# Performance work log

Hardware: AMD Instinct MI355X
Metric: run time of the kernel (lower is better)

Reference implementation:

```python
import jax, jax.numpy as jnp
import numpy as np

N_SEND = 49152   # 12 * 64^2 HEALPix nodes
N_REC = 65536    # 256x256 receiver grid
N_EDGES = 262144 # N_REC * 4 nearest senders
D_MODEL = 256
EDGE_IN, EDGE_OUT = 4, 64
LIN_IN, LIN_OUT = 320, 256
B = 2


def setup_inputs() -> dict:
    key = jax.random.key(0)
    ks = jax.random.split(key, 8)
    x = jax.random.normal(ks[0], (B, N_SEND, D_MODEL), dtype=jnp.float32)
    senders = jax.random.randint(ks[1], (N_EDGES,), 0, N_SEND, dtype=jnp.int32)
    receivers = jax.random.randint(ks[2], (N_EDGES,), 0, N_REC, dtype=jnp.int32)
    edge_index = jnp.stack([senders, receivers], axis=0)
    edge_attr = jax.random.normal(ks[3], (N_EDGES, EDGE_IN), dtype=jnp.float32)
    s = lambda fan_in: 1.0 / np.sqrt(fan_in)
    return {
        "x": x,
        "edge_index": edge_index,
        "edge_attr": edge_attr,
        "ee_w1": jax.random.normal(ks[4], (EDGE_IN, EDGE_OUT), dtype=jnp.float32) * s(EDGE_IN),
        "ee_b1": jnp.zeros((EDGE_OUT,), dtype=jnp.float32),
        "ee_w2": jax.random.normal(ks[5], (EDGE_OUT, EDGE_OUT), dtype=jnp.float32) * s(EDGE_OUT),
        "ee_b2": jnp.zeros((EDGE_OUT,), dtype=jnp.float32),
        "ff_w1": jax.random.normal(ks[6], (LIN_IN, LIN_OUT), dtype=jnp.float32) * s(LIN_IN),
        "ff_b1": jnp.zeros((LIN_OUT,), dtype=jnp.float32),
        "ff_w2": jax.random.normal(ks[7], (LIN_OUT, LIN_OUT), dtype=jnp.float32) * s(LIN_OUT),
        "ff_b2": jnp.zeros((LIN_OUT,), dtype=jnp.float32),
    }


def reference(x, edge_index, edge_attr,
              ee_w1, ee_b1, ee_w2, ee_b2,
              ff_w1, ff_b1, ff_w2, ff_b2):
    senders, receivers = edge_index[0], edge_index[1]
    # edge embedder MLP: [E, edge_in] -> [E, edge_out]
    h = jax.nn.relu(edge_attr @ ee_w1 + ee_b1)
    edge_feat = h @ ee_w2 + ee_b2                       # [E, edge_out]
    # gather sender node features: [B, E, d_model]
    v_s = x[:, senders, :]
    # concat with broadcast edge features: [B, E, d_model + edge_out]
    ef = jnp.broadcast_to(edge_feat[None], (x.shape[0],) + edge_feat.shape)
    v_s_prime = jnp.concatenate([v_s, ef], axis=-1)
    # scatter-sum onto receiver nodes: [B, n_rec, lin_in]
    v_m_sum = jnp.zeros((x.shape[0], N_REC, v_s_prime.shape[-1]), dtype=x.dtype)
    v_m_sum = v_m_sum.at[:, receivers, :].add(v_s_prime)
    # g2m feedforward: [B, n_rec, lin_out]
    h2 = jax.nn.relu(v_m_sum @ ff_w1 + ff_b1)
    return h2 @ ff_w2 + ff_b2
```

## Files before the change

### kernel.cpp

```cpp
#include <hip/hip_runtime.h>
#include <hip/hip_bf16.h>

#define N_SEND 49152
#define N_REC  65536
#define N_EDGES 262144
#define D_MODEL 256
#define EDGE_IN 4
#define EDGE_OUT 64
#define LIN_IN 320
#define LIN_OUT 256
#define BATCH 2

#define EPB 32
#define GBM 128

typedef __attribute__((ext_vector_type(4))) float f32x4;
typedef __attribute__((ext_vector_type(8))) short bf16x8;

static __device__ __forceinline__ unsigned short f2bf(float f) {
    union { float f; unsigned u; } v; v.f = f;
    unsigned r = v.u + 0x7FFF + ((v.u >> 16) & 1);
    return (unsigned short)(r >> 16);
}
static __device__ __forceinline__ float bf2f(unsigned short h) {
    union { unsigned u; float f; } v; v.u = ((unsigned)h) << 16; return v.f;
}

static __device__ __forceinline__ void async_copy16(void* lds_ptr, const void* g_ptr) {
    __builtin_amdgcn_global_load_lds(
        (const __attribute__((address_space(1))) void*)g_ptr,
        (__attribute__((address_space(3))) void*)lds_ptr, 16, 0, 0);
}

__global__ __launch_bounds__(256) void conv_x_kernel(
    const float* __restrict__ x, unsigned short* __restrict__ xb)
{
    const size_t i = ((size_t)blockIdx.x * 256 + threadIdx.x) * 8;
    const float4 v0 = *(const float4*)&x[i];
    const float4 v1 = *(const float4*)&x[i + 4];
    bf16x8 o;
    o[0] = (short)f2bf(v0.x); o[1] = (short)f2bf(v0.y);
    o[2] = (short)f2bf(v0.z); o[3] = (short)f2bf(v0.w);
    o[4] = (short)f2bf(v1.x); o[5] = (short)f2bf(v1.y);
    o[6] = (short)f2bf(v1.z); o[7] = (short)f2bf(v1.w);
    *(bf16x8*)&xb[i] = o;
}

__global__ __launch_bounds__(256) void edge_mlp_kernel(
    const int* __restrict__ receivers,
    const float* __restrict__ edge_attr,
    const float* __restrict__ ee_w1, const float* __restrict__ ee_b1,
    const float* __restrict__ ee_w2, const float* __restrict__ ee_b2,
    unsigned short* __restrict__ efs, int* __restrict__ counts)
{
    __shared__ float h_lds[EPB][EDGE_OUT];
    __shared__ float e_lds[EPB][EDGE_OUT];

    const int tid = threadIdx.x;
    const int e0 = blockIdx.x * EPB;

    if (tid < EPB) atomicAdd(&counts[receivers[e0 + tid]], 1);

    for (int i = tid; i < EPB * EDGE_OUT; i += 256) {
        const int e = i >> 6, j = i & 63;
        const float* ea = edge_attr + (size_t)(e0 + e) * EDGE_IN;
        float acc = ee_b1[j];
        acc += ea[0] * ee_w1[0 * EDGE_OUT + j];
        acc += ea[1] * ee_w1[1 * EDGE_OUT + j];
        acc += ea[2] * ee_w1[2 * EDGE_OUT + j];
        acc += ea[3] * ee_w1[3 * EDGE_OUT + j];
        h_lds[e][j] = fmaxf(acc, 0.0f);
    }
    __syncthreads();

    {
        const int j = tid & 63, g = tid >> 6;
        float acc[8];
#pragma unroll
        for (int e = 0; e < 8; ++e) acc[e] = ee_b2[j];
        for (int k = 0; k < EDGE_OUT; ++k) {
            const float w = ee_w2[k * EDGE_OUT + j];
#pragma unroll
            for (int e = 0; e < 8; ++e) acc[e] += h_lds[g * 8 + e][k] * w;
        }
#pragma unroll
        for (int e = 0; e < 8; ++e) e_lds[g * 8 + e][j] = acc[e];
    }
    __syncthreads();

    {
        const int e = tid >> 3, seg = tid & 7;
        const float* src = &e_lds[e][seg * 8];
        bf16x8 o;
#pragma unroll
        for (int j = 0; j < 8; ++j) o[j] = (short)f2bf(src[j]);
        *(bf16x8*)&efs[(size_t)(e0 + e) * EDGE_OUT + seg * 8] = o;
    }
}

__global__ __launch_bounds__(1024) void scan_kernel(
    const int* __restrict__ counts, int* __restrict__ row_ptr,
    int* __restrict__ cursor)
{
    __shared__ int sums[1024];
    const int t = threadIdx.x;
    const int4* c4 = (const int4*)(counts + t * 64);

    int s = 0;
#pragma unroll
    for (int i = 0; i < 16; ++i) { const int4 c = c4[i]; s += c.x + c.y + c.z + c.w; }
    sums[t] = s;
    __syncthreads();

    for (int off = 1; off < 1024; off <<= 1) {
        const int v = (t >= off) ? sums[t - off] : 0;
        __syncthreads();
        sums[t] += v;
        __syncthreads();
    }

    int run = sums[t] - s;
#pragma unroll
    for (int i = 0; i < 16; ++i) {
        const int4 c = c4[i];
        int4 w;
        w.x = run; w.y = run + c.x; w.z = w.y + c.y; w.w = w.z + c.z;
        run = w.w + c.w;
        ((int4*)(row_ptr + t * 64))[i] = w;
        ((int4*)(cursor + t * 64))[i] = w;
    }
    if (t == 1023) row_ptr[N_REC] = run;
}

__global__ __launch_bounds__(256) void fill_kernel(
    const int* __restrict__ senders, const int* __restrict__ receivers,
    int* __restrict__ cursor, int* __restrict__ edge_order,
    int* __restrict__ ssort)
{
    const int e = blockIdx.x * 256 + threadIdx.x;
    const int r = receivers[e];
    const int pos = atomicAdd(&cursor[r], 1);
    edge_order[pos] = e;
    ssort[pos] = senders[e];
}

template<bool XB>
__global__ __launch_bounds__(256) void gather_kernel(
    const float* __restrict__ x,
    const unsigned short* __restrict__ xb,
    const unsigned short* __restrict__ efs,
    const int* __restrict__ row_ptr,
    const int* __restrict__ edge_order,
    const int* __restrict__ ssort,
    unsigned short* __restrict__ vmb)
{
    const int lane = threadIdx.x & 63;
    const int wave = threadIdx.x >> 6;
    const int r = blockIdx.x * 4 + wave;
    const int beg = row_ptr[r], end = row_ptr[r + 1];
    const int half = lane >> 5, l2 = lane & 31;

    float ax[8] = {0, 0, 0, 0, 0, 0, 0, 0};
    float ae[8] = {0, 0, 0, 0, 0, 0, 0, 0};

    for (int chunk = beg; chunk < end; chunk += 64) {
        const int n = min(64, end - chunk);
        int myidx = 0, myeidx = 0;
        if (chunk + lane < end) {
            myidx = ssort[chunk + lane];
            myeidx = edge_order[chunk + lane];
        }
        for (int i = 0; i < n; ++i) {
            const int s = __shfl(myidx, i);
            const int e = __shfl(myeidx, i);
            const size_t rowbase = (size_t)(half ? N_SEND + s : s) * D_MODEL;
            if (XB) {
                const bf16x8 v = *(const bf16x8*)&xb[rowbase + l2 * 8];
#pragma unroll
                for (int j = 0; j < 8; ++j) ax[j] += bf2f((unsigned short)v[j]);
            } else {
                const float4 v0 = *(const float4*)&x[rowbase + l2 * 8];
                const float4 v1 = *(const float4*)&x[rowbase + l2 * 8 + 4];
                ax[0] += v0.x; ax[1] += v0.y; ax[2] += v0.z; ax[3] += v0.w;
                ax[4] += v1.x; ax[5] += v1.y; ax[6] += v1.z; ax[7] += v1.w;
            }
            if (lane < 8) {
                const bf16x8 w = *(const bf16x8*)&efs[(size_t)e * EDGE_OUT + lane * 8];
#pragma unroll
                for (int j = 0; j < 8; ++j) ae[j] += bf2f((unsigned short)w[j]);
            }
        }
    }

    bf16x8 o;
#pragma unroll
    for (int j = 0; j < 8; ++j) o[j] = (short)f2bf(ax[j]);
    *(bf16x8*)&vmb[((size_t)(half * N_REC + r)) * LIN_IN + l2 * 8] = o;
    if (lane < 8) {
        bf16x8 oe;
#pragma unroll
        for (int j = 0; j < 8; ++j) oe[j] = (short)f2bf(ae[j]);
        *(bf16x8*)&vmb[((size_t)r) * LIN_IN + D_MODEL + lane * 8] = oe;
        *(bf16x8*)&vmb[((size_t)(N_REC + r)) * LIN_IN + D_MODEL + lane * 8] = oe;
    }
}

__global__ __launch_bounds__(256) void prep_weights(
    const float* __restrict__ w1, const float* __restrict__ w2,
    unsigned short* __restrict__ w1t, unsigned short* __restrict__ w2t)
{
    const int tid = blockIdx.x * 256 + threadIdx.x;
    if (tid < 256 * LIN_IN) {
        const int n = tid / LIN_IN, k = tid - n * LIN_IN;
        w1t[tid] = f2bf(w1[k * LIN_OUT + n]);
    } else {
        const int t2 = tid - 256 * LIN_IN;
        if (t2 < 256 * 256) {
            const int n = t2 >> 8, k = t2 & 255;
            w2t[t2] = f2bf(w2[k * LIN_OUT + n]);
        }
    }
}

template<int K, bool IS_L1>
__global__ __launch_bounds__(512, 2) void gemm_node(
    const unsigned short* __restrict__ A,
    const unsigned short* __restrict__ BT,
    const float* __restrict__ bias,
    unsigned short* __restrict__ hout,
    float* __restrict__ fout)
{
    __shared__ __align__(16) char lds[49152];

    const int tid  = threadIdx.x;
    const int lane = tid & 63, wave = tid >> 6;
    const int n16  = lane & 15, hi = lane >> 4;
    const int wr   = wave >> 2, wc = wave & 3;
    const size_t row0 = (size_t)blockIdx.x * GBM;

    const int f_l = (n16 & 3) ^ ((n16 >> 2) & 3);
    const int hsl = (hi ^ f_l) << 4;

    auto stage = [&](int kk, int buf) {
        {
            const int i = tid, row = i >> 2;
            const int sl = (i & 3) ^ ((row & 3) ^ ((row >> 2) & 3));
            const unsigned short* g = A + (row0 + row) * LIN_IN + kk + sl * 8;
            char* l = lds + (buf << 13) + ((tid >> 6) << 10);
            async_copy16(l, g);
        }
#pragma unroll
        for (int p = 0; p < 2; ++p) {
            const int i = p * 512 + tid, row = i >> 2;
            const int sl = (i & 3) ^ ((row & 3) ^ ((row >> 2) & 3));
            const unsigned short* g = BT + (size_t)row * K + kk + sl * 8;
            char* l = lds + 16384 + (buf << 14) + (p << 13) + ((tid >> 6) << 10);
            async_copy16(l, g);
        }
    };

    f32x4 acc[4][4];
#pragma unroll
    for (int c = 0; c < 4; ++c) {
        const float bv = bias[64 * wc + 16 * c + n16];
#pragma unroll
        for (int t = 0; t < 4; ++t) {
            acc[t][c][0] = bv; acc[t][c][1] = bv; acc[t][c][2] = bv; acc[t][c][3] = bv;
        }
    }

    stage(0, 0);
    int cur = 0;
    const int NSTEP = K / 32;
    for (int step = 0; step < NSTEP; ++step) {
        if (step + 1 < NSTEP) stage((step + 1) * 32, cur ^ 1);
        __syncthreads();

        bf16x8 af[4], bf[4];
        const char* Ab = lds + (cur << 13);
        const char* Bb = lds + 16384 + (cur << 14);
#pragma unroll
        for (int t = 0; t < 4; ++t)
            af[t] = *(const bf16x8*)(Ab + (64 * wr + 16 * t + n16) * 64 + hsl);
#pragma unroll
        for (int c = 0; c < 4; ++c)
            bf[c] = *(const bf16x8*)(Bb + (64 * wc + 16 * c + n16) * 64 + hsl);
#pragma unroll
        for (int c = 0; c < 4; ++c)
#pragma unroll
            for (int t = 0; t < 4; ++t)
                acc[t][c] = __builtin_amdgcn_mfma_f32_16x16x32_bf16(af[t], bf[c], acc[t][c], 0, 0, 0);

        __syncthreads();
        cur ^= 1;
    }

    if (IS_L1) {
#pragma unroll
        for (int t = 0; t < 4; ++t)
#pragma unroll
            for (int c = 0; c < 4; ++c)
#pragma unroll
                for (int r = 0; r < 4; ++r)
                    hout[(row0 + 64 * wr + 16 * t + 4 * hi + r) * LIN_IN + 64 * wc + 16 * c + n16] =
                        f2bf(fmaxf(acc[t][c][r], 0.0f));
    } else {
#pragma unroll
        for (int t = 0; t < 4; ++t)
#pragma unroll
            for (int c = 0; c < 4; ++c)
#pragma unroll
                for (int r = 0; r < 4; ++r)
                    fout[(row0 + 64 * wr + 16 * t + 4 * hi + r) * LIN_OUT + 64 * wc + 16 * c + n16] =
                        acc[t][c][r];
    }
}

extern "C" void kernel_launch(void* const* d_in, const int* in_sizes, int n_in,
                              void* d_out, int out_size, void* d_ws, size_t ws_size,
                              hipStream_t stream) {
    const float* x         = (const float*)d_in[0];
    const int*   edge_idx  = (const int*)d_in[1];
    const float* edge_attr = (const float*)d_in[2];
    const float* ee_w1     = (const float*)d_in[3];
    const float* ee_b1     = (const float*)d_in[4];
    const float* ee_w2     = (const float*)d_in[5];
    const float* ee_b2     = (const float*)d_in[6];
    const float* ff_w1     = (const float*)d_in[7];
    const float* ff_b1     = (const float*)d_in[8];
    const float* ff_w2     = (const float*)d_in[9];
    const float* ff_b2     = (const float*)d_in[10];
    float* out = (float*)d_out;

    const int* senders   = edge_idx;
    const int* receivers = edge_idx + N_EDGES;

    char* ws = (char*)d_ws;
    size_t off = 0;
    auto alloc = [&](size_t bytes) { char* p = ws + off; off += (bytes + 511) & ~511ull; return p; };

    unsigned short* vmb = (unsigned short*)alloc((size_t)BATCH * N_REC * LIN_IN * 2);
    unsigned short* efs = (unsigned short*)alloc((size_t)N_EDGES * EDGE_OUT * 2);
    unsigned short* w1t = (unsigned short*)alloc((size_t)256 * LIN_IN * 2);
    unsigned short* w2t = (unsigned short*)alloc((size_t)256 * LIN_OUT * 2);
    int* row_ptr        = (int*)alloc((size_t)(N_REC + 1) * 4);
    int* counts         = (int*)alloc((size_t)N_REC * 4);
    int* cursor         = (int*)alloc((size_t)N_REC * 4);
    int* edge_order     = (int*)alloc((size_t)N_EDGES * 4);
    int* ssort          = (int*)alloc((size_t)N_EDGES * 4);
    const size_t base_need = off;
    unsigned short* xb  = (unsigned short*)(ws + off);
    const size_t xb_bytes = (size_t)BATCH * N_SEND * D_MODEL * 2;
    const bool use_xb = (ws_size >= base_need + xb_bytes);

    hipMemsetAsync(counts, 0, (size_t)N_REC * 4, stream);

    prep_weights<<<(256 * LIN_IN + 256 * LIN_OUT + 255) / 256, 256, 0, stream>>>(
        ff_w1, ff_w2, w1t, w2t);

    if (use_xb) {
        conv_x_kernel<<<(int)((size_t)BATCH * N_SEND * D_MODEL / 8 / 256), 256, 0, stream>>>(x, xb);
    }

    edge_mlp_kernel<<<N_EDGES / EPB, 256, 0, stream>>>(
        receivers, edge_attr, ee_w1, ee_b1, ee_w2, ee_b2, efs, counts);

    scan_kernel<<<1, 1024, 0, stream>>>(counts, row_ptr, cursor);

    fill_kernel<<<N_EDGES / 256, 256, 0, stream>>>(
        senders, receivers, cursor, edge_order, ssort);

    if (use_xb) {
        gather_kernel<true><<<N_REC / 4, 256, 0, stream>>>(
            x, xb, efs, row_ptr, edge_order, ssort, vmb);
    } else {
        gather_kernel<false><<<N_REC / 4, 256, 0, stream>>>(
            x, xb, efs, row_ptr, edge_order, ssort, vmb);
    }

    const int ngrid = (BATCH * N_REC) / GBM;
    gemm_node<LIN_IN, true><<<ngrid, 512, 0, stream>>>(vmb, w1t, ff_b1, vmb, nullptr);
    gemm_node<LIN_OUT, false><<<ngrid, 512, 0, stream>>>(vmb, w2t, ff_b2, nullptr, out);
}
```

Baseline: 285.6 us.

## Fuse node MLP GEMMs via LDS-resident hidden tile and merge prep kernels

Merges the two node-feedforward GEMMs into one kernel: the ReLU'd bf16 hidden tile (128x256) is written into a swizzled LDS region and used directly as the A operand of the second GEMM, removing the global round-trip of the hidden activations. It also folds the x conversion, edge MLP, and weight transpose into a single launch by partitioning block IDs. The fused GEMM needs 112KB of LDS and occupancy drops to one block per CU, which may reduce latency hiding.

```diff
diff --git a/kernel.cpp b/kernel.cpp
--- a/kernel.cpp
+++ b/kernel.cpp
@@ -32,69 +32,90 @@
         (__attribute__((address_space(3))) void*)lds_ptr, 16, 0, 0);
 }
 
-__global__ __launch_bounds__(256) void conv_x_kernel(
-    const float* __restrict__ x, unsigned short* __restrict__ xb)
-{
-    const size_t i = ((size_t)blockIdx.x * 256 + threadIdx.x) * 8;
-    const float4 v0 = *(const float4*)&x[i];
-    const float4 v1 = *(const float4*)&x[i + 4];
-    bf16x8 o;
-    o[0] = (short)f2bf(v0.x); o[1] = (short)f2bf(v0.y);
-    o[2] = (short)f2bf(v0.z); o[3] = (short)f2bf(v0.w);
-    o[4] = (short)f2bf(v1.x); o[5] = (short)f2bf(v1.y);
-    o[6] = (short)f2bf(v1.z); o[7] = (short)f2bf(v1.w);
-    *(bf16x8*)&xb[i] = o;
-}
-
-__global__ __launch_bounds__(256) void edge_mlp_kernel(
-    const int* __restrict__ receivers,
-    const float* __restrict__ edge_attr,
+__global__ __launch_bounds__(256) void prep_fused(
+    const float* __restrict__ x, unsigned short* __restrict__ xb, int nconv,
+    const int* __restrict__ receivers, const float* __restrict__ edge_attr,
     const float* __restrict__ ee_w1, const float* __restrict__ ee_b1,
     const float* __restrict__ ee_w2, const float* __restrict__ ee_b2,
-    unsigned short* __restrict__ efs, int* __restrict__ counts)
+    unsigned short* __restrict__ efs, int* __restrict__ counts,
+    const float* __restrict__ w1, const float* __restrict__ w2,
+    unsigned short* __restrict__ w1t, unsigned short* __restrict__ w2t)
 {
     __shared__ float h_lds[EPB][EDGE_OUT];
     __shared__ float e_lds[EPB][EDGE_OUT];
 
+    const int bid = blockIdx.x;
     const int tid = threadIdx.x;
-    const int e0 = blockIdx.x * EPB;
-
-    if (tid < EPB) atomicAdd(&counts[receivers[e0 + tid]], 1);
-
-    for (int i = tid; i < EPB * EDGE_OUT; i += 256) {
-        const int e = i >> 6, j = i & 63;
-        const float* ea = edge_attr + (size_t)(e0 + e) * EDGE_IN;
-        float acc = ee_b1[j];
-        acc += ea[0] * ee_w1[0 * EDGE_OUT + j];
-        acc += ea[1] * ee_w1[1 * EDGE_OUT + j];
-        acc += ea[2] * ee_w1[2 * EDGE_OUT + j];
-        acc += ea[3] * ee_w1[3 * EDGE_OUT + j];
-        h_lds[e][j] = fmaxf(acc, 0.0f);
-    }
-    __syncthreads();
+
+    if (bid < nconv) {
+        const size_t i = ((size_t)bid * 256 + tid) * 8;
+        const float4 v0 = *(const float4*)&x[i];
+        const float4 v1 = *(const float4*)&x[i + 4];
+        bf16x8 o;
+        o[0] = (short)f2bf(v0.x); o[1] = (short)f2bf(v0.y);
+        o[2] = (short)f2bf(v0.z); o[3] = (short)f2bf(v0.w);
+        o[4] = (short)f2bf(v1.x); o[5] = (short)f2bf(v1.y);
+        o[6] = (short)f2bf(v1.z); o[7] = (short)f2bf(v1.w);
+        *(bf16x8*)&xb[i] = o;
+        return;
+    }
+    const int b2 = bid - nconv;
+
+    if (b2 < N_EDGES / EPB) {
+        const int e0 = b2 * EPB;
+
+        if (tid < EPB) atomicAdd(&counts[receivers[e0 + tid]], 1);
+
+        for (int i = tid; i < EPB * EDGE_OUT; i += 256) {
+            const int e = i >> 6, j = i & 63;
+            const float* ea = edge_attr + (size_t)(e0 + e) * EDGE_IN;
+            float acc = ee_b1[j];
+            acc += ea[0] * ee_w1[0 * EDGE_OUT + j];
+            acc += ea[1] * ee_w1[1 * EDGE_OUT + j];
+            acc += ea[2] * ee_w1[2 * EDGE_OUT + j];
+            acc += ea[3] * ee_w1[3 * EDGE_OUT + j];
+            h_lds[e][j] = fmaxf(acc, 0.0f);
+        }
+        __syncthreads();
+
+        {
+            const int j = tid & 63, g = tid >> 6;
+            float acc[8];
+#pragma unroll
+            for (int e = 0; e < 8; ++e) acc[e] = ee_b2[j];
+            for (int k = 0; k < EDGE_OUT; ++k) {
+                const float w = ee_w2[k * EDGE_OUT + j];
+#pragma unroll
+                for (int e = 0; e < 8; ++e) acc[e] += h_lds[g * 8 + e][k] * w;
+            }
+#pragma unroll
+            for (int e = 0; e < 8; ++e) e_lds[g * 8 + e][j] = acc[e];
+        }
+        __syncthreads();
+
+        {
+            const int e = tid >> 3, seg = tid & 7;
+            const float* src = &e_lds[e][seg * 8];
+            bf16x8 o;
+#pragma unroll
+            for (int j = 0; j < 8; ++j) o[j] = (short)f2bf(src[j]);
+            *(bf16x8*)&efs[(size_t)(e0 + e) * EDGE_OUT + seg * 8] = o;
+        }
+        return;
+    }
 
     {
-        const int j = tid & 63, g = tid >> 6;
-        float acc[8];
-#pragma unroll
-        for (int e = 0; e < 8; ++e) acc[e] = ee_b2[j];
-        for (int k = 0; k < EDGE_OUT; ++k) {
-            const float w = ee_w2[k * EDGE_OUT + j];
-#pragma unroll
-            for (int e = 0; e < 8; ++e) acc[e] += h_lds[g * 8 + e][k] * w;
-        }
-#pragma unroll
-        for (int e = 0; e < 8; ++e) e_lds[g * 8 + e][j] = acc[e];
-    }
-    __syncthreads();
-
-    {
-        const int e = tid >> 3, seg = tid & 7;
-        const float* src = &e_lds[e][seg * 8];
-        bf16x8 o;
-#pragma unroll
-        for (int j = 0; j < 8; ++j) o[j] = (short)f2bf(src[j]);
-        *(bf16x8*)&efs[(size_t)(e0 + e) * EDGE_OUT + seg * 8] = o;
+        const int t3 = (b2 - N_EDGES / EPB) * 256 + tid;
+        if (t3 < 256 * LIN_IN) {
+            const int n = t3 / LIN_IN, k = t3 - n * LIN_IN;
+            w1t[t3] = f2bf(w1[k * LIN_OUT + n]);
+        } else {
+            const int t2 = t3 - 256 * LIN_IN;
+            if (t2 < 256 * 256) {
+                const int n = t2 >> 8, k = t2 & 255;
+                w2t[t2] = f2bf(w2[k * LIN_OUT + n]);
+            }
+        }
     }
 }
 
@@ -205,55 +226,39 @@
     }
 }
 
-__global__ __launch_bounds__(256) void prep_weights(
-    const float* __restrict__ w1, const float* __restrict__ w2,
-    unsigned short* __restrict__ w1t, unsigned short* __restrict__ w2t)
+__global__ __launch_bounds__(512, 1) void node_mlp_fused(
+    const unsigned short* __restrict__ vmb,
+    const unsigned short* __restrict__ w1t,
+    const float* __restrict__ b1,
+    const unsigned short* __restrict__ w2t,
+    const float* __restrict__ b2,
+    float* __restrict__ out)
 {
-    const int tid = blockIdx.x * 256 + threadIdx.x;
-    if (tid < 256 * LIN_IN) {
-        const int n = tid / LIN_IN, k = tid - n * LIN_IN;
-        w1t[tid] = f2bf(w1[k * LIN_OUT + n]);
-    } else {
-        const int t2 = tid - 256 * LIN_IN;
-        if (t2 < 256 * 256) {
-            const int n = t2 >> 8, k = t2 & 255;
-            w2t[t2] = f2bf(w2[k * LIN_OUT + n]);
-        }
-    }
-}
-
-template<int K, bool IS_L1>
-__global__ __launch_bounds__(512, 2) void gemm_node(
-    const unsigned short* __restrict__ A,
-    const unsigned short* __restrict__ BT,
-    const float* __restrict__ bias,
-    unsigned short* __restrict__ hout,
-    float* __restrict__ fout)
-{
-    __shared__ __align__(16) char lds[49152];
+    __shared__ __align__(16) char lds[114688];
 
     const int tid  = threadIdx.x;
     const int lane = tid & 63, wave = tid >> 6;
     const int n16  = lane & 15, hi = lane >> 4;
     const int wr   = wave >> 2, wc = wave & 3;
     const size_t row0 = (size_t)blockIdx.x * GBM;
+    char* const hbase = lds + 49152;
 
     const int f_l = (n16 & 3) ^ ((n16 >> 2) & 3);
     const int hsl = (hi ^ f_l) << 4;
 
-    auto stage = [&](int kk, int buf) {
-        {
-            const int i = tid, row = i >> 2;
-            const int sl = (i & 3) ^ ((row & 3) ^ ((row >> 2) & 3));
-            const unsigned short* g = A + (row0 + row) * LIN_IN + kk + sl * 8;
-            char* l = lds + (buf << 13) + ((tid >> 6) << 10);
-            async_copy16(l, g);
-        }
+    auto stageA = [&](int kk, int buf) {
+        const int row = tid >> 2;
+        const int sl = (tid & 3) ^ ((row & 3) ^ ((row >> 2) & 3));
+        const unsigned short* g = vmb + (row0 + row) * LIN_IN + kk + sl * 8;
+        char* l = lds + (buf << 13) + ((tid >> 6) << 10);
+        async_copy16(l, g);
+    };
+    auto stageB = [&](const unsigned short* BT, int ldk, int kk, int buf) {
 #pragma unroll
         for (int p = 0; p < 2; ++p) {
             const int i = p * 512 + tid, row = i >> 2;
             const int sl = (i & 3) ^ ((row & 3) ^ ((row >> 2) & 3));
-            const unsigned short* g = BT + (size_t)row * K + kk + sl * 8;
+            const unsigned short* g = BT + (size_t)row * ldk + kk + sl * 8;
             char* l = lds + 16384 + (buf << 14) + (p << 13) + ((tid >> 6) << 10);
             async_copy16(l, g);
         }
@@ -262,18 +267,20 @@
     f32x4 acc[4][4];
 #pragma unroll
     for (int c = 0; c < 4; ++c) {
-        const float bv = bias[64 * wc + 16 * c + n16];
+        const float bv = b1[64 * wc + 16 * c + n16];
 #pragma unroll
         for (int t = 0; t < 4; ++t) {
             acc[t][c][0] = bv; acc[t][c][1] = bv; acc[t][c][2] = bv; acc[t][c][3] = bv;
         }
     }
 
-    stage(0, 0);
+    stageA(0, 0); stageB(w1t, LIN_IN, 0, 0);
     int cur = 0;
-    const int NSTEP = K / 32;
-    for (int step = 0; step < NSTEP; ++step) {
-        if (step + 1 < NSTEP) stage((step + 1) * 32, cur ^ 1);
+    for (int step = 0; step < LIN_IN / 32; ++step) {
+        if (step + 1 < LIN_IN / 32) {
+            stageA((step + 1) * 32, cur ^ 1);
+            stageB(w1t, LIN_IN, (step + 1) * 32, cur ^ 1);
+        }
         __syncthreads();
 
         bf16x8 af[4], bf[4];
@@ -295,25 +302,67 @@
         cur ^= 1;
     }
 
-    if (IS_L1) {
+#pragma unroll
+    for (int t = 0; t < 4; ++t)
+#pragma unroll
+        for (int c = 0; c < 4; ++c) {
+            const int col = 64 * wc + 16 * c + n16;
+            const int kc = col >> 5;
+            const int b  = (col & 31) * 2;
+            const int gslot = b >> 4;
+#pragma unroll
+            for (int r = 0; r < 4; ++r) {
+                const int lrow = 64 * wr + 16 * t + 4 * hi + r;
+                const int f = (lrow & 3) ^ ((lrow >> 2) & 3);
+                *(unsigned short*)(hbase + (kc << 13) + lrow * 64 + (((gslot ^ f) << 4) | (b & 15))) =
+                    f2bf(fmaxf(acc[t][c][r], 0.0f));
+            }
+        }
+    __syncthreads();
+
+    f32x4 acc2[4][4];
+#pragma unroll
+    for (int c = 0; c < 4; ++c) {
+        const float bv = b2[64 * wc + 16 * c + n16];
+#pragma unroll
+        for (int t = 0; t < 4; ++t) {
+            acc2[t][c][0] = bv; acc2[t][c][1] = bv; acc2[t][c][2] = bv; acc2[t][c][3] = bv;
+        }
+    }
+
+    stageB(w2t, LIN_OUT, 0, 0);
+    cur = 0;
+    for (int step = 0; step < LIN_OUT / 32; ++step) {
+        if (step + 1 < LIN_OUT / 32) stageB(w2t, LIN_OUT, (step + 1) * 32, cur ^ 1);
+        __syncthreads();
+
+        bf16x8 af[4], bf[4];
+        const char* Hb = hbase + (step << 13);
+        const char* Bb = lds + 16384 + (cur << 14);
 #pragma unroll
         for (int t = 0; t < 4; ++t)
-#pragma unroll
-            for (int c = 0; c < 4; ++c)
-#pragma unroll
-                for (int r = 0; r < 4; ++r)
-                    hout[(row0 + 64 * wr + 16 * t + 4 * hi + r) * LIN_IN + 64 * wc + 16 * c + n16] =
-                        f2bf(fmaxf(acc[t][c][r], 0.0f));
-    } else {
-#pragma unroll
-        for (int t = 0; t < 4; ++t)
-#pragma unroll
-            for (int c = 0; c < 4; ++c)
-#pragma unroll
-                for (int r = 0; r < 4; ++r)
-                    fout[(row0 + 64 * wr + 16 * t + 4 * hi + r) * LIN_OUT + 64 * wc + 16 * c + n16] =
-                        acc[t][c][r];
-    }
+            af[t] = *(const bf16x8*)(Hb + (64 * wr + 16 * t + n16) * 64 + hsl);
+#pragma unroll
+        for (int c = 0; c < 4; ++c)
+            bf[c] = *(const bf16x8*)(Bb + (64 * wc + 16 * c + n16) * 64 + hsl);
+#pragma unroll
+        for (int c = 0; c < 4; ++c)
+#pragma unroll
+            for (int t = 0; t < 4; ++t)
+                acc2[t][c] = __builtin_amdgcn_mfma_f32_16x16x32_bf16(af[t], bf[c], acc2[t][c], 0, 0, 0);
+
+        __syncthreads();
+        cur ^= 1;
+    }
+
+#pragma unroll
+    for (int t = 0; t < 4; ++t)
+#pragma unroll
+        for (int c = 0; c < 4; ++c)
+#pragma unroll
+            for (int r = 0; r < 4; ++r)
+                out[(row0 + 64 * wr + 16 * t + 4 * hi + r) * LIN_OUT + 64 * wc + 16 * c + n16] =
+                    acc2[t][c][r];
 }
 
 extern "C" void kernel_launch(void* const* d_in, const int* in_sizes, int n_in,
@@ -355,15 +404,11 @@
 
     hipMemsetAsync(counts, 0, (size_t)N_REC * 4, stream);
 
-    prep_weights<<<(256 * LIN_IN + 256 * LIN_OUT + 255) / 256, 256, 0, stream>>>(
-        ff_w1, ff_w2, w1t, w2t);
-
-    if (use_xb) {
-        conv_x_kernel<<<(int)((size_t)BATCH * N_SEND * D_MODEL / 8 / 256), 256, 0, stream>>>(x, xb);
-    }
-
-    edge_mlp_kernel<<<N_EDGES / EPB, 256, 0, stream>>>(
-        receivers, edge_attr, ee_w1, ee_b1, ee_w2, ee_b2, efs, counts);
+    const int nconv = use_xb ? (int)((size_t)BATCH * N_SEND * D_MODEL / 8 / 256) : 0;
+    const int prep_grid = nconv + N_EDGES / EPB + (256 * LIN_IN + 256 * LIN_OUT + 255) / 256;
+    prep_fused<<<prep_grid, 256, 0, stream>>>(
+        x, xb, nconv, receivers, edge_attr, ee_w1, ee_b1, ee_w2, ee_b2,
+        efs, counts, ff_w1, ff_w2, w1t, w2t);
 
     scan_kernel<<<1, 1024, 0, stream>>>(counts, row_ptr, cursor);
 
@@ -378,7 +423,6 @@
             x, xb, efs, row_ptr, edge_order, ssort, vmb);
     }
 
-    const int ngrid = (BATCH * N_REC) / GBM;
-    gemm_node<LIN_IN, true><<<ngrid, 512, 0, stream>>>(vmb, w1t, ff_b1, vmb, nullptr);
-    gemm_node<LIN_OUT, false><<<ngrid, 512, 0, stream>>>(vmb, w2t, ff_b2, nullptr, out);
-}
+    node_mlp_fused<<<(BATCH * N_REC) / GBM, 512, 0, stream>>>(
+        vmb, w1t, ff_b1, w2t, ff_b2, out);
+}
```

New measurement: 285.2 us. About the same (-0.2%).
